# Optimization experiments

Measured on AMD Instinct MI355X. Metric: run time of the kernel, lower is better.

The kernel has to match this reference:

```python
import jax, jax.numpy as jnp
import numpy as np

B, V, H, W = 2, 4, 352, 352
R_PIX = H * W
SH_DEGREE = 1
D_SH = (SH_DEGREE + 1) ** 2
SCALE_MIN, SCALE_MAX = 0.5, 15.0
EPS = 1e-8
C0 = 0.28209479177387814  # SH DC basis constant


def quat_to_mat(q):
    # (w, x, y, z) convention, matches pytorch3d quaternion_to_matrix
    w, x, y, z = q[..., 0], q[..., 1], q[..., 2], q[..., 3]
    two_s = 2.0 / jnp.sum(q * q, axis=-1)
    o = jnp.stack([
        1 - two_s * (y * y + z * z), two_s * (x * y - z * w), two_s * (x * z + y * w),
        two_s * (x * y + z * w), 1 - two_s * (x * x + z * z), two_s * (y * z - x * w),
        two_s * (x * z - y * w), two_s * (y * z + x * w), 1 - two_s * (x * x + y * y),
    ], axis=-1)
    return o.reshape(*q.shape[:-1], 3, 3)


def setup_inputs() -> dict:
    key = jax.random.key(0)
    ks = jax.random.split(key, 8)
    # valid c2w extrinsics: random rotation (from unit quaternion) + translation
    q = jax.random.normal(ks[0], (B, V, 4))
    q = q / jnp.linalg.norm(q, axis=-1, keepdims=True)
    Rm = quat_to_mat(q)
    t = jax.random.normal(ks[1], (B, V, 3))
    E = jnp.zeros((B, V, 4, 4))
    E = E.at[..., :3, :3].set(Rm).at[..., :3, 3].set(t).at[..., 3, 3].set(1.0)
    extrinsics = E.reshape(B, V, 1, 1, 1, 4, 4)
    # normalized pinhole intrinsics
    f = jax.random.uniform(ks[2], (B, V, 2), minval=0.8, maxval=1.2)
    K = jnp.zeros((B, V, 3, 3))
    K = K.at[..., 0, 0].set(f[..., 0]).at[..., 1, 1].set(f[..., 1])
    K = K.at[..., 0, 2].set(0.5).at[..., 1, 2].set(0.5).at[..., 2, 2].set(1.0)
    intrinsics = K.reshape(B, V, 1, 1, 1, 3, 3)
    coordinates = jax.random.uniform(ks[3], (B, V, R_PIX, 1, 1, 2))
    depths = jax.random.uniform(ks[4], (B, V, R_PIX, 1, 1), minval=0.5, maxval=10.0)
    opacities = jax.random.uniform(ks[5], (B, V, R_PIX, 1, 1))
    raw_gaussians = jax.random.normal(ks[6], (B, V, R_PIX, 1, 1, 7 + 3 * D_SH))
    input_images = jax.random.uniform(ks[7], (B, V, 3, H, W))
    sh_mask = jnp.ones((D_SH,), jnp.float32)
    for deg in range(1, SH_DEGREE + 1):
        sh_mask = sh_mask.at[deg ** 2:(deg + 1) ** 2].set(0.1 * 0.25 ** deg)
    return {"extrinsics": extrinsics, "intrinsics": intrinsics, "coordinates": coordinates,
            "depths": depths, "opacities": opacities, "raw_gaussians": raw_gaussians,
            "input_images": input_images, "sh_mask": sh_mask}


def reference(extrinsics, intrinsics, coordinates, depths, opacities, raw_gaussians, input_images, sh_mask):
    d_sh = sh_mask.shape[0]
    # split raw gaussians: scales (3), quaternion (4), sh (3*d_sh)
    scales = jnp.clip(jax.nn.softplus(raw_gaussians[..., :3] - 4.0), SCALE_MIN, SCALE_MAX)
    rot = raw_gaussians[..., 3:7]
    rotations = rot / (jnp.linalg.norm(rot, axis=-1, keepdims=True) + EPS)
    sh = raw_gaussians[..., 7:].reshape(*raw_gaussians.shape[:-1], 3, d_sh) * sh_mask
    # inject image colors into the DC SH coefficient
    b, v, c, h, w = input_images.shape
    imgs = input_images.transpose(0, 1, 3, 4, 2).reshape(b, v, h * w, 1, 1, c)
    sh = sh.at[..., 0].add((imgs - 0.5) / C0)  # RGB2SH
    # covariance = R diag(s^2) R^T, then rotate into world frame
    Rq = quat_to_mat(rotations)
    cov = jnp.einsum('...ij,...j,...kj->...ik', Rq, scales * scales, Rq)
    Rc = extrinsics[..., :3, :3]  # (b,v,1,1,1,3,3) c2w rotation
    cov = jnp.einsum('...ij,...jk,...lk->...il', Rc, cov, Rc)
    # unproject rays: d = normalize(K^-1 [x,y,1]), world dir = R d, origin = t
    Kinv = jnp.linalg.inv(intrinsics)
    xy1 = jnp.concatenate([coordinates, jnp.ones_like(coordinates[..., :1])], axis=-1)
    d = jnp.einsum('...ij,...j->...i', Kinv, xy1)
    d = d / jnp.linalg.norm(d, axis=-1, keepdims=True)
    dirs = jnp.einsum('...ij,...j->...i', Rc, d)
    means = jnp.broadcast_to(extrinsics[..., :3, 3], dirs.shape) + dirs * depths[..., None]
    # rotate SH: degree 0 identity; degree 1 Wigner-D = P R P^T with P: (x,y,z)->(y,z,x)
    perm = jnp.array([1, 2, 0])
    D1 = Rc[..., perm[:, None], perm[None, :]]  # (b,v,1,1,1,3,3)
    sh1 = jnp.einsum('...ij,...xj->...xi', D1, sh[..., 1:4])
    harmonics = jnp.concatenate([sh[..., :1], sh1], axis=-1)
    return means, cov, scales, rotations, harmonics, opacities
```

## Files before the change

### kernel.cpp

```cpp
#include <hip/hip_runtime.h>

#define R_PIX 123904
#define NVIEW 8
#define NPIX  (R_PIX * (size_t)NVIEW)

#define OFF_MEANS  ((size_t)0)
#define OFF_COV    ((size_t)(3  * NPIX))
#define OFF_SCALES ((size_t)(12 * NPIX))
#define OFF_ROT    ((size_t)(15 * NPIX))
#define OFF_HARM   ((size_t)(19 * NPIX))
#define OFF_OPAC   ((size_t)(31 * NPIX))

#define SLICE_DW 1216
#define LDS_DW   (SLICE_DW * 4)

typedef float f4v __attribute__((ext_vector_type(4)));

__device__ __forceinline__ void nt_store4(float* p, float x, float y, float z, float w) {
    f4v v = { x, y, z, w };
    __builtin_nontemporal_store(v, (f4v*)p);
}
__device__ __forceinline__ void nt_store4(float* p, const float4& v) {
    nt_store4(p, v.x, v.y, v.z, v.w);
}

__device__ __forceinline__ void g2lds16(const void* g, void* l) {
    __builtin_amdgcn_global_load_lds(
        (__attribute__((address_space(1))) void*)g,
        (__attribute__((address_space(3))) void*)l,
        16, 0, 0);
}

__device__ __forceinline__ void lds_fence() {
    asm volatile("s_waitcnt lgkmcnt(0)" ::: "memory");
}

__global__ __launch_bounds__(256) void gaussian_adapter_kernel(
    const float* __restrict__ extr,
    const float* __restrict__ intr,
    const float* __restrict__ coords,
    const float* __restrict__ depths,
    const float* __restrict__ opac,
    const float* __restrict__ raw,
    const float* __restrict__ imgs,
    const float* __restrict__ shmask,
    float* __restrict__ out)
{
    const int t    = threadIdx.x;
    const int lane = t & 63;
    const int w    = t >> 6;
    const int bv   = blockIdx.y;
    const int bp0  = blockIdx.x * 256;
    const size_t base_pix = (size_t)bv * R_PIX + bp0;
    const int p   = bp0 + t;
    const size_t pix = base_pix + t;

    __shared__ __align__(16) float lds[LDS_DW];
    float* slice = lds + w * SLICE_DW;

    {
        const float4* g = (const float4*)(raw + base_pix * 19) + w * 304;
        #pragma unroll
        for (int r = 0; r < 4; r++)
            g2lds16(g + r * 64 + lane, (char*)slice + r * 1024);
        g2lds16(g + 240 + lane, (char*)slice + 3840);
    }

    float Rc[3][3], tvec[3];
    {
        const float* E = extr + bv * 16;
        #pragma unroll
        for (int i = 0; i < 3; i++) {
            #pragma unroll
            for (int j = 0; j < 3; j++) Rc[i][j] = E[i * 4 + j];
            tvec[i] = E[i * 4 + 3];
        }
    }
    const float* K = intr + bv * 9;
    const float fx = K[0], cx = K[2];
    const float fy = K[4], cy = K[5];
    const float sm0 = shmask[0], sm1 = shmask[1], sm2 = shmask[2], sm3 = shmask[3];

    const float2 uv  = ((const float2*)coords)[pix];
    const float  dep = depths[pix];
    const float  op  = opac[pix];
    float im[3];
    #pragma unroll
    for (int c = 0; c < 3; c++)
        im[c] = imgs[((size_t)bv * 3 + c) * R_PIX + p];

    __syncthreads();

    const float* my = lds + t * 19;

    float rg[19];
    #pragma unroll
    for (int i = 0; i < 19; i++) rg[i] = my[i];

    const float LOG2E = 1.4426950408889634f;
    const float LN2   = 0.6931471805599453f;
    float sc[3];
    #pragma unroll
    for (int k = 0; k < 3; k++) {
        float xv = rg[k] - 4.0f;
        float e  = __builtin_amdgcn_exp2f(-fabsf(xv) * LOG2E);
        float sp = fmaxf(xv, 0.0f) + LN2 * __builtin_amdgcn_logf(1.0f + e);
        sc[k] = fminf(fmaxf(sp, 0.5f), 15.0f);
    }

    float q0 = rg[3], q1 = rg[4], q2 = rg[5], q3 = rg[6];
    {
        const float qn = q0 * q0 + q1 * q1 + q2 * q2 + q3 * q3;
        const float inorm = __builtin_amdgcn_rsqf(qn);
        q0 *= inorm; q1 *= inorm; q2 *= inorm; q3 *= inorm;
    }

    const float two_s = 2.0f;
    float Rq[3][3];
    Rq[0][0] = 1.0f - two_s * (q2 * q2 + q3 * q3);
    Rq[0][1] = two_s * (q1 * q2 - q3 * q0);
    Rq[0][2] = two_s * (q1 * q3 + q2 * q0);
    Rq[1][0] = two_s * (q1 * q2 + q3 * q0);
    Rq[1][1] = 1.0f - two_s * (q1 * q1 + q3 * q3);
    Rq[1][2] = two_s * (q2 * q3 - q1 * q0);
    Rq[2][0] = two_s * (q1 * q3 - q2 * q0);
    Rq[2][1] = two_s * (q2 * q3 + q1 * q0);
    Rq[2][2] = 1.0f - two_s * (q1 * q1 + q2 * q2);

    const float s2[3] = { sc[0] * sc[0], sc[1] * sc[1], sc[2] * sc[2] };
    float cov3[3][3];
    #pragma unroll
    for (int i = 0; i < 3; i++)
        #pragma unroll
        for (int k = 0; k < 3; k++)
            cov3[i][k] = Rq[i][0] * s2[0] * Rq[k][0]
                       + Rq[i][1] * s2[1] * Rq[k][1]
                       + Rq[i][2] * s2[2] * Rq[k][2];
    float cov[3][3];
    #pragma unroll
    for (int i = 0; i < 3; i++) {
        float m0 = Rc[i][0] * cov3[0][0] + Rc[i][1] * cov3[1][0] + Rc[i][2] * cov3[2][0];
        float m1 = Rc[i][0] * cov3[0][1] + Rc[i][1] * cov3[1][1] + Rc[i][2] * cov3[2][1];
        float m2 = Rc[i][0] * cov3[0][2] + Rc[i][1] * cov3[1][2] + Rc[i][2] * cov3[2][2];
        #pragma unroll
        for (int l = 0; l < 3; l++)
            cov[i][l] = m0 * Rc[l][0] + m1 * Rc[l][1] + m2 * Rc[l][2];
    }

    float means[3];
    {
        const float rfx = __builtin_amdgcn_rcpf(fx);
        const float rfy = __builtin_amdgcn_rcpf(fy);
        float d0 = (uv.x - cx) * rfx;
        float d1 = (uv.y - cy) * rfy;
        const float rn = __builtin_amdgcn_rsqf(d0 * d0 + d1 * d1 + 1.0f);
        d0 *= rn; d1 *= rn;
        const float d2 = rn;
        #pragma unroll
        for (int i = 0; i < 3; i++)
            means[i] = tvec[i] + (Rc[i][0] * d0 + Rc[i][1] * d1 + Rc[i][2] * d2) * dep;
    }

    float harm[3][4];
    {
        const float invC0 = 1.0f / 0.28209479177387814f;
        const int perm[3] = {1, 2, 0};
        #pragma unroll
        for (int c = 0; c < 3; c++) {
            float s1  = rg[7 + c * 4 + 1] * sm1;
            float s2v = rg[7 + c * 4 + 2] * sm2;
            float s3  = rg[7 + c * 4 + 3] * sm3;
            harm[c][0] = rg[7 + c * 4] * sm0 + (im[c] - 0.5f) * invC0;
            #pragma unroll
            for (int i = 0; i < 3; i++)
                harm[c][1 + i] = Rc[perm[i]][perm[0]] * s1
                               + Rc[perm[i]][perm[1]] * s2v
                               + Rc[perm[i]][perm[2]] * s3;
        }
    }

    nt_store4(out + OFF_ROT + pix * 4, q0, q1, q2, q3);
    __builtin_nontemporal_store(op, out + OFF_OPAC + pix);

    const size_t wpix = base_pix + (size_t)(w * 64);
    float* means_g = out + OFF_MEANS  + wpix * 3;
    float* cov_g   = out + OFF_COV    + wpix * 9;
    float* sc_g    = out + OFF_SCALES + wpix * 3;
    float* hm_g    = out + OFF_HARM   + wpix * 12;

    lds_fence();
    #pragma unroll
    for (int i = 0; i < 3; i++) slice[lane * 3 + i] = means[i];
    #pragma unroll
    for (int i = 0; i < 3; i++)
        #pragma unroll
        for (int j = 0; j < 3; j++) slice[192 + lane * 9 + i * 3 + j] = cov[i][j];
    #pragma unroll
    for (int i = 0; i < 3; i++) slice[768 + lane * 3 + i] = sc[i];

    lds_fence();

    {
        const float4* sv = (const float4*)slice;
        float4 v0 = sv[lane];
        if (lane < 48) nt_store4(means_g + 4 * lane, v0);
        else           nt_store4(cov_g + 4 * (lane - 48), v0);
        float4 v1 = sv[lane + 64];
        nt_store4(cov_g + 4 * (lane + 16), v1);
        float4 v2 = sv[lane + 128];
        nt_store4(cov_g + 4 * (lane + 80), v2);
        if (lane < 48) {
            float4 v3 = sv[lane + 192];
            nt_store4(sc_g + 4 * lane, v3);
        }
    }

    lds_fence();
    #pragma unroll
    for (int c = 0; c < 3; c++)
        #pragma unroll
        for (int j = 0; j < 4; j++) slice[lane * 13 + c * 4 + j] = harm[c][j];

    lds_fence();

    #pragma unroll
    for (int it = 0; it < 3; it++) {
        const int i = lane + 64 * it;
        const int px = i / 3, k = i % 3;
        const float* s = slice + px * 13 + k * 4;
        nt_store4(hm_g + 4 * i, s[0], s[1], s[2], s[3]);
    }
}

extern "C" void kernel_launch(void* const* d_in, const int* in_sizes, int n_in,
                              void* d_out, int out_size, void* d_ws, size_t ws_size,
                              hipStream_t stream) {
    const float* extr   = (const float*)d_in[0];
    const float* intr   = (const float*)d_in[1];
    const float* coords = (const float*)d_in[2];
    const float* depths = (const float*)d_in[3];
    const float* opac   = (const float*)d_in[4];
    const float* raw    = (const float*)d_in[5];
    const float* imgs   = (const float*)d_in[6];
    const float* shmask = (const float*)d_in[7];
    float* out = (float*)d_out;

    dim3 grid(R_PIX / 256, NVIEW);
    dim3 block(256);
    gaussian_adapter_kernel<<<grid, block, 0, stream>>>(
        extr, intr, coords, depths, opac, raw, imgs, shmask, out);
}
```

Before: 223.4 us.

## Drop LDS staging; load raw params and store outputs directly per thread

```diff
diff --git a/kernel.cpp b/kernel.cpp
--- a/kernel.cpp
+++ b/kernel.cpp
@@ -1,4 +1,5 @@
 #include <hip/hip_runtime.h>
+
 
 #define R_PIX 123904
 #define NVIEW 8
@@ -11,28 +12,12 @@
 #define OFF_HARM   ((size_t)(19 * NPIX))
 #define OFF_OPAC   ((size_t)(31 * NPIX))
 
-#define SLICE_DW 1216
-#define LDS_DW   (SLICE_DW * 4)
-
 typedef float f4v __attribute__((ext_vector_type(4)));
+typedef float f4u __attribute__((ext_vector_type(4), aligned(4)));
 
 __device__ __forceinline__ void nt_store4(float* p, float x, float y, float z, float w) {
     f4v v = { x, y, z, w };
     __builtin_nontemporal_store(v, (f4v*)p);
-}
-__device__ __forceinline__ void nt_store4(float* p, const float4& v) {
-    nt_store4(p, v.x, v.y, v.z, v.w);
-}
-
-__device__ __forceinline__ void g2lds16(const void* g, void* l) {
-    __builtin_amdgcn_global_load_lds(
-        (__attribute__((address_space(1))) void*)g,
-        (__attribute__((address_space(3))) void*)l,
-        16, 0, 0);
-}
-
-__device__ __forceinline__ void lds_fence() {
-    asm volatile("s_waitcnt lgkmcnt(0)" ::: "memory");
 }
 
 __global__ __launch_bounds__(256) void gaussian_adapter_kernel(
@@ -46,25 +31,27 @@
     const float* __restrict__ shmask,
     float* __restrict__ out)
 {
-    const int t    = threadIdx.x;
-    const int lane = t & 63;
-    const int w    = t >> 6;
-    const int bv   = blockIdx.y;
-    const int bp0  = blockIdx.x * 256;
+    const int t   = threadIdx.x;
+    const int bv  = blockIdx.y;
+    const int bp0 = blockIdx.x * 256;
     const size_t base_pix = (size_t)bv * R_PIX + bp0;
     const int p   = bp0 + t;
     const size_t pix = base_pix + t;
 
-    __shared__ __align__(16) float lds[LDS_DW];
-    float* slice = lds + w * SLICE_DW;
-
-    {
-        const float4* g = (const float4*)(raw + base_pix * 19) + w * 304;
-        #pragma unroll
-        for (int r = 0; r < 4; r++)
-            g2lds16(g + r * 64 + lane, (char*)slice + r * 1024);
-        g2lds16(g + 240 + lane, (char*)slice + 3840);
-    }
+    const float* rp = raw + pix * 19;
+    const f4u r0 = *(const f4u*)(rp);
+    const f4u r1 = *(const f4u*)(rp + 4);
+    const f4u r2 = *(const f4u*)(rp + 8);
+    const f4u r3 = *(const f4u*)(rp + 12);
+    const float r16 = rp[16], r17 = rp[17], r18 = rp[18];
+
+    const float2 uv  = ((const float2*)coords)[pix];
+    const float  dep = depths[pix];
+    const float  op  = opac[pix];
+    float im[3];
+    #pragma unroll
+    for (int c = 0; c < 3; c++)
+        im[c] = imgs[((size_t)bv * 3 + c) * R_PIX + p];
 
     float Rc[3][3], tvec[3];
     {
@@ -81,21 +68,11 @@
     const float fy = K[4], cy = K[5];
     const float sm0 = shmask[0], sm1 = shmask[1], sm2 = shmask[2], sm3 = shmask[3];
 
-    const float2 uv  = ((const float2*)coords)[pix];
-    const float  dep = depths[pix];
-    const float  op  = opac[pix];
-    float im[3];
-    #pragma unroll
-    for (int c = 0; c < 3; c++)
-        im[c] = imgs[((size_t)bv * 3 + c) * R_PIX + p];
-
-    __syncthreads();
-
-    const float* my = lds + t * 19;
-
-    float rg[19];
-    #pragma unroll
-    for (int i = 0; i < 19; i++) rg[i] = my[i];
+    float rg[19] = { r0.x, r0.y, r0.z, r0.w,
+                     r1.x, r1.y, r1.z, r1.w,
+                     r2.x, r2.y, r2.z, r2.w,
+                     r3.x, r3.y, r3.z, r3.w,
+                     r16, r17, r18 };
 
     const float LOG2E = 1.4426950408889634f;
     const float LN2   = 0.6931471805599453f;
@@ -180,55 +157,30 @@
     }
 
     nt_store4(out + OFF_ROT + pix * 4, q0, q1, q2, q3);
+    {
+        float* g = out + OFF_HARM + pix * 12;
+        nt_store4(g,     harm[0][0], harm[0][1], harm[0][2], harm[0][3]);
+        nt_store4(g + 4, harm[1][0], harm[1][1], harm[1][2], harm[1][3]);
+        nt_store4(g + 8, harm[2][0], harm[2][1], harm[2][2], harm[2][3]);
+    }
     __builtin_nontemporal_store(op, out + OFF_OPAC + pix);
 
-    const size_t wpix = base_pix + (size_t)(w * 64);
-    float* means_g = out + OFF_MEANS  + wpix * 3;
-    float* cov_g   = out + OFF_COV    + wpix * 9;
-    float* sc_g    = out + OFF_SCALES + wpix * 3;
-    float* hm_g    = out + OFF_HARM   + wpix * 12;
-
-    lds_fence();
-    #pragma unroll
-    for (int i = 0; i < 3; i++) slice[lane * 3 + i] = means[i];
-    #pragma unroll
-    for (int i = 0; i < 3; i++)
-        #pragma unroll
-        for (int j = 0; j < 3; j++) slice[192 + lane * 9 + i * 3 + j] = cov[i][j];
-    #pragma unroll
-    for (int i = 0; i < 3; i++) slice[768 + lane * 3 + i] = sc[i];
-
-    lds_fence();
-
-    {
-        const float4* sv = (const float4*)slice;
-        float4 v0 = sv[lane];
-        if (lane < 48) nt_store4(means_g + 4 * lane, v0);
-        else           nt_store4(cov_g + 4 * (lane - 48), v0);
-        float4 v1 = sv[lane + 64];
-        nt_store4(cov_g + 4 * (lane + 16), v1);
-        float4 v2 = sv[lane + 128];
-        nt_store4(cov_g + 4 * (lane + 80), v2);
-        if (lane < 48) {
-            float4 v3 = sv[lane + 192];
-            nt_store4(sc_g + 4 * lane, v3);
-        }
-    }
-
-    lds_fence();
-    #pragma unroll
-    for (int c = 0; c < 3; c++)
-        #pragma unroll
-        for (int j = 0; j < 4; j++) slice[lane * 13 + c * 4 + j] = harm[c][j];
-
-    lds_fence();
-
-    #pragma unroll
-    for (int it = 0; it < 3; it++) {
-        const int i = lane + 64 * it;
-        const int px = i / 3, k = i % 3;
-        const float* s = slice + px * 13 + k * 4;
-        nt_store4(hm_g + 4 * i, s[0], s[1], s[2], s[3]);
+    {
+        float* g = out + OFF_MEANS + pix * 3;
+        #pragma unroll
+        for (int i = 0; i < 3; i++) g[i] = means[i];
+    }
+    {
+        float* g = out + OFF_COV + pix * 9;
+        #pragma unroll
+        for (int i = 0; i < 3; i++)
+            #pragma unroll
+            for (int j = 0; j < 3; j++) g[i * 3 + j] = cov[i][j];
+    }
+    {
+        float* g = out + OFF_SCALES + pix * 3;
+        #pragma unroll
+        for (int i = 0; i < 3; i++) g[i] = sc[i];
     }
 }
 
```

Result: slower. 228.2 us (+2.1%).
